# Optimization experiments

Hardware: AMD Instinct MI355X
Metric: run time of the kernel (lower is better)

The kernel has to match this reference:

```python
import jax, jax.numpy as jnp
import numpy as np

B, T, C = 256, 512, 128


def setup_inputs() -> dict:
    key = jax.random.key(0)
    k1, k2, k3 = jax.random.split(key, 3)
    inputs = jax.random.normal(k1, (B, T, C), dtype=jnp.float32)
    # learned transition matrix (orthogonal init approximated by scaled normal)
    transitions = jax.random.normal(k2, (C, C), dtype=jnp.float32) * 0.1
    # variable sequence lengths in [T//2, T] -> keras-style boolean mask
    lengths = jax.random.randint(k3, (B,), T // 2, T + 1)
    mask = jnp.arange(T)[None, :] < lengths[:, None]  # [B, T] bool
    return {"inputs": inputs, "mask": mask, "transitions": transitions}


def reference(inputs, mask, transitions):
    # Faithful port of CRF.call: sequence_lengths from mask, then Viterbi decode
    # (tfa.text.crf_decode): max-plus forward DP with backpointers + backtrack.
    Bn, Tn, Cn = inputs.shape
    seq_len = jnp.sum(mask.astype(jnp.int32), axis=-1)  # [B]

    ident = jnp.arange(Cn, dtype=jnp.int32)[None, :]  # identity backpointer row

    def fwd_step(state, xs):
        # state: [B, C] best score ending in each tag
        pot_t, valid = xs  # [B, C], [B] bool
        scores = state[:, :, None] + transitions[None]      # [B, Cprev, Ccur]
        new_state = jnp.max(scores, axis=1) + pot_t          # [B, C]
        bp = jnp.argmax(scores, axis=1).astype(jnp.int32)    # [B, C]
        state = jnp.where(valid[:, None], new_state, state)  # carry past length
        bp = jnp.where(valid[:, None], bp, ident)            # identity beyond length
        return state, bp

    pots = jnp.swapaxes(inputs[:, 1:], 0, 1)  # [T-1, B, C]
    valid = mask[:, 1:].T                      # [T-1, B]
    state, bps = jax.lax.scan(fwd_step, inputs[:, 0], (pots, valid))

    last_tag = jnp.argmax(state, axis=-1).astype(jnp.int32)  # [B]

    def bwd_step(tag, bp_t):
        prev = jnp.take_along_axis(bp_t, tag[:, None], axis=1)[:, 0]
        return prev, prev

    _, tags_rest = jax.lax.scan(bwd_step, last_tag, bps, reverse=True)  # [T-1, B]
    viterbi = jnp.concatenate([tags_rest, last_tag[None]], axis=0).T    # [B, T]
    return viterbi, inputs, seq_len, transitions
```

## Files before the change

### kernel.cpp

```cpp
#include <hip/hip_runtime.h>


#define BB 256
#define TT 512
#define CC 128
#define NTH 1024
#define GR 8
#define JP 16
#define SPAD 20

#define OFF_VIT 0
#define OFF_INP (BB * TT)
#define OFF_LEN (OFF_INP + BB * TT * CC)
#define OFF_TR (OFF_LEN + BB)

#define BP_BYTES ((TT - 1) * CC)
#define STATE_FLOATS (2 * GR * SPAD)
#define SMEM_BYTES (BP_BYTES + STATE_FLOATS * 4 + 16 * 4 + 16)

template <int CTRL>
__device__ __forceinline__ void dpp_first_max(float& v, int& bi) {
  float ov = __int_as_float(__builtin_amdgcn_update_dpp(0, __float_as_int(v), CTRL, 0xF, 0xF, true));
  int oi = __builtin_amdgcn_update_dpp(0, bi, CTRL, 0xF, 0xF, true);
  bool take = (ov > v) || (ov == v && oi < bi);
  v = take ? ov : v;
  bi = take ? oi : bi;
}

#define CHAIN(VNAME, JIDX, BACC, IACC)              \
  {                                                 \
    float VNAME = sjv + tr[JIDX];                   \
    if (VNAME > BACC) { BACC = VNAME; IACC = JIDX; } \
  }

__global__ __launch_bounds__(NTH, 1) void crf_viterbi(
    const float* __restrict__ inputs, const unsigned char* __restrict__ mask_bytes,
    const float* __restrict__ trans, float* __restrict__ out) {
  extern __shared__ unsigned char smem[];
  unsigned char* bp_s = smem;
  float* state_s = (float*)(smem + BP_BYTES);
  int* wsum = (int*)(state_s + STATE_FLOATS);

  const int b = blockIdx.x;
  const int tid = threadIdx.x;
  const int lane = tid & 63;
  const int wave = tid >> 6;
  const int ccur = tid >> 3;
  const int g = tid & 7;

  const int w4 = (mask_bytes[1] == 0) ? 4 : 1;
  if (tid < TT) {
    int mb = mask_bytes[(size_t)(b * TT + tid) * (size_t)w4] != 0;
    unsigned long long bal = __ballot(mb);
    if (lane == 0) wsum[wave] = __popcll(bal);
  }

  float tr[JP];
#pragma unroll
  for (int j = 0; j < JP; ++j) tr[j] = trans[(g * JP + j) * CC + ccur];

  const float* pin = inputs + (size_t)b * TT * CC;

  if (tid < CC) state_s[(tid >> 4) * SPAD + (tid & 15)] = pin[tid];
  __syncthreads();

  int L = 0;
#pragma unroll
  for (int i = 0; i < 8; ++i) L += wsum[i];

  float pot = pin[CC + ccur];
  int par = 0;

  for (int t = 1; t < L; ++t) {
    const float4* sp = (const float4*)(state_s + par * (GR * SPAD) + g * SPAD);
    float4 a0 = sp[0], a1 = sp[1], a2 = sp[2], a3 = sp[3];

    int tn = (t + 1 < L) ? (t + 1) : t;
    float potN = pin[tn * CC + ccur];

    float b0 = a0.x + tr[0]; int i0 = 0;
    float b1 = a0.y + tr[1]; int i1 = 1;
    { float sjv = a0.z; CHAIN(v2, 2, b0, i0) }
    { float sjv = a0.w; CHAIN(v3, 3, b1, i1) }
    { float sjv = a1.x; CHAIN(v4, 4, b0, i0) }
    { float sjv = a1.y; CHAIN(v5, 5, b1, i1) }
    { float sjv = a1.z; CHAIN(v6, 6, b0, i0) }
    { float sjv = a1.w; CHAIN(v7, 7, b1, i1) }
    { float sjv = a2.x; CHAIN(v8, 8, b0, i0) }
    { float sjv = a2.y; CHAIN(v9, 9, b1, i1) }
    { float sjv = a2.z; CHAIN(vA, 10, b0, i0) }
    { float sjv = a2.w; CHAIN(vB, 11, b1, i1) }
    { float sjv = a3.x; CHAIN(vC, 12, b0, i0) }
    { float sjv = a3.y; CHAIN(vD, 13, b1, i1) }
    { float sjv = a3.z; CHAIN(vE, 14, b0, i0) }
    { float sjv = a3.w; CHAIN(vF, 15, b1, i1) }

    bool t1 = (b1 > b0) || (b1 == b0 && i1 < i0);
    float v = t1 ? b1 : b0;
    int bi = (t1 ? i1 : i0) + g * JP;

    dpp_first_max<0xB1>(v, bi);
    dpp_first_max<0x4E>(v, bi);
    dpp_first_max<0x141>(v, bi);

    v += pot;

    if (g == 0) {
      state_s[(par ^ 1) * (GR * SPAD) + (ccur >> 4) * SPAD + (ccur & 15)] = v;
      bp_s[(t - 1) * CC + ccur] = (unsigned char)bi;
    }
    pot = potN;
    __syncthreads();
    par ^= 1;
  }

  if (wave == 0) {
    const float* fs = state_s + par * (GR * SPAD);
    float v1 = fs[(lane >> 4) * SPAD + (lane & 15)];
    int c2 = lane + 64;
    float v2 = fs[(c2 >> 4) * SPAD + (c2 & 15)];
    float v;
    int idx;
    if (v2 > v1) { v = v2; idx = c2; } else { v = v1; idx = lane; }
#pragma unroll
    for (int off = 32; off; off >>= 1) {
      float ov = __shfl_xor(v, off);
      int oi = __shfl_xor(idx, off);
      if (ov > v || (ov == v && oi < idx)) { v = ov; idx = oi; }
    }
    for (int t2 = L - 1 + lane; t2 < TT; t2 += 64) out[OFF_VIT + b * TT + t2] = (float)idx;
    if (lane == 0) {
      int cur = idx;
      for (int tt = L - 2; tt >= 0; --tt) {
        cur = bp_s[tt * CC + cur];
        out[OFF_VIT + b * TT + tt] = (float)cur;
      }
      out[OFF_LEN + b] = (float)L;
    }
  } else {
    if (wave == 1) out[OFF_TR + b * 64 + lane] = trans[b * 64 + lane];
    const float4* src = (const float4*)pin;
    float4* dst = (float4*)(out + OFF_INP + (size_t)b * TT * CC);
    for (int i = tid - 64; i < TT * CC / 4; i += NTH - 64) dst[i] = src[i];
  }
}

extern "C" void kernel_launch(void* const* d_in, const int* in_sizes, int n_in,
                              void* d_out, int out_size, void* d_ws, size_t ws_size,
                              hipStream_t stream) {
  const float* inputs = (const float*)d_in[0];
  const unsigned char* mask = (const unsigned char*)d_in[1];
  const float* trans = (const float*)d_in[2];
  float* out = (float*)d_out;

  crf_viterbi<<<BB, NTH, SMEM_BYTES, stream>>>(inputs, mask, trans, out);
}
```

Measured before the change: 501.9 us.

## Drop backpointer argmax from forward pass; recompute path from stored scores

The forward DP now computes only the max over previous tags, with no argmax index tracking. Each step's state vector goes to a global history buffer (workspace, or the output's input slot as fallback). The backtrack recomputes each argmax from the stored scores plus a transposed transition matrix in shared memory, using a wave-wide butterfly, and prefetches history rows ahead. This shortens the serial per-step critical path at the cost of global writes every step and a heavier serial backtrack. It also replaces __syncthreads with a raw lgkmcnt wait plus barrier.

```diff
diff --git a/kernel.cpp b/kernel.cpp
--- a/kernel.cpp
+++ b/kernel.cpp
@@ -14,31 +14,45 @@
 #define OFF_LEN (OFF_INP + BB * TT * CC)
 #define OFF_TR (OFF_LEN + BB)
 
-#define BP_BYTES ((TT - 1) * CC)
+#define TRT_FLOATS (CC * CC)
 #define STATE_FLOATS (2 * GR * SPAD)
-#define SMEM_BYTES (BP_BYTES + STATE_FLOATS * 4 + 16 * 4 + 16)
+#define SMEM_BYTES ((TRT_FLOATS + STATE_FLOATS + 16) * 4 + 16)
 
-template <int CTRL>
-__device__ __forceinline__ void dpp_first_max(float& v, int& bi) {
-  float ov = __int_as_float(__builtin_amdgcn_update_dpp(0, __float_as_int(v), CTRL, 0xF, 0xF, true));
-  int oi = __builtin_amdgcn_update_dpp(0, bi, CTRL, 0xF, 0xF, true);
-  bool take = (ov > v) || (ov == v && oi < bi);
-  v = take ? ov : v;
-  bi = take ? oi : bi;
+#define F3(a, b, c) fmaxf(fmaxf((a), (b)), (c))
+
+template <int C>
+__device__ __forceinline__ float dppmaxf(float v) {
+  float o = __int_as_float(__builtin_amdgcn_update_dpp(0, __float_as_int(v), C, 0xF, 0xF, true));
+  return fmaxf(v, o);
 }
 
-#define CHAIN(VNAME, JIDX, BACC, IACC)              \
-  {                                                 \
-    float VNAME = sjv + tr[JIDX];                   \
-    if (VNAME > BACC) { BACC = VNAME; IACC = JIDX; } \
-  }
+__device__ __forceinline__ void lexmax(float& v, int& i, float ov, int oi) {
+  bool take = (ov > v) || (ov == v && oi < i);
+  v = take ? ov : v;
+  i = take ? oi : i;
+}
+template <int C>
+__device__ __forceinline__ void bfly_dpp(float& v, int& i) {
+  float ov = __int_as_float(__builtin_amdgcn_update_dpp(0, __float_as_int(v), C, 0xF, 0xF, true));
+  int oi = __builtin_amdgcn_update_dpp(0, i, C, 0xF, 0xF, true);
+  lexmax(v, i, ov, oi);
+}
+__device__ __forceinline__ void bfly6(float& v, int& i) {
+  bfly_dpp<0xB1>(v, i);
+  bfly_dpp<0x4E>(v, i);
+  bfly_dpp<0x141>(v, i);
+  bfly_dpp<0x140>(v, i);
+  { float ov = __shfl_xor(v, 16); int oi = __shfl_xor(i, 16); lexmax(v, i, ov, oi); }
+  { float ov = __shfl_xor(v, 32); int oi = __shfl_xor(i, 32); lexmax(v, i, ov, oi); }
+}
 
 __global__ __launch_bounds__(NTH, 1) void crf_viterbi(
     const float* __restrict__ inputs, const unsigned char* __restrict__ mask_bytes,
-    const float* __restrict__ trans, float* __restrict__ out) {
-  extern __shared__ unsigned char smem[];
-  unsigned char* bp_s = smem;
-  float* state_s = (float*)(smem + BP_BYTES);
+    const float* __restrict__ trans, float* __restrict__ out,
+    float* __restrict__ hist, int useWs) {
+  extern __shared__ float smemf[];
+  float* trT = smemf;
+  float* state_s = smemf + TRT_FLOATS;
   int* wsum = (int*)(state_s + STATE_FLOATS);
 
   const int b = blockIdx.x;
@@ -55,13 +69,32 @@
     if (lane == 0) wsum[wave] = __popcll(bal);
   }
 
+  {
+    const float4* tsrc = (const float4*)(trans + tid * 16);
+    float4 q0 = tsrc[0], q1 = tsrc[1], q2 = tsrc[2], q3 = tsrc[3];
+    int p = tid >> 3, c0 = (tid & 7) * 16;
+    trT[(c0 + 0) * CC + p] = q0.x;  trT[(c0 + 1) * CC + p] = q0.y;
+    trT[(c0 + 2) * CC + p] = q0.z;  trT[(c0 + 3) * CC + p] = q0.w;
+    trT[(c0 + 4) * CC + p] = q1.x;  trT[(c0 + 5) * CC + p] = q1.y;
+    trT[(c0 + 6) * CC + p] = q1.z;  trT[(c0 + 7) * CC + p] = q1.w;
+    trT[(c0 + 8) * CC + p] = q2.x;  trT[(c0 + 9) * CC + p] = q2.y;
+    trT[(c0 + 10) * CC + p] = q2.z; trT[(c0 + 11) * CC + p] = q2.w;
+    trT[(c0 + 12) * CC + p] = q3.x; trT[(c0 + 13) * CC + p] = q3.y;
+    trT[(c0 + 14) * CC + p] = q3.z; trT[(c0 + 15) * CC + p] = q3.w;
+  }
+
   float tr[JP];
 #pragma unroll
   for (int j = 0; j < JP; ++j) tr[j] = trans[(g * JP + j) * CC + ccur];
 
   const float* pin = inputs + (size_t)b * TT * CC;
+  float* hist_b = hist + (size_t)b * TT * CC;
 
-  if (tid < CC) state_s[(tid >> 4) * SPAD + (tid & 15)] = pin[tid];
+  if (tid < CC) {
+    float x0 = pin[tid];
+    state_s[(tid >> 4) * SPAD + (tid & 15)] = x0;
+    hist_b[tid] = x0;
+  }
   __syncthreads();
 
   int L = 0;
@@ -78,66 +111,66 @@
     int tn = (t + 1 < L) ? (t + 1) : t;
     float potN = pin[tn * CC + ccur];
 
-    float b0 = a0.x + tr[0]; int i0 = 0;
-    float b1 = a0.y + tr[1]; int i1 = 1;
-    { float sjv = a0.z; CHAIN(v2, 2, b0, i0) }
-    { float sjv = a0.w; CHAIN(v3, 3, b1, i1) }
-    { float sjv = a1.x; CHAIN(v4, 4, b0, i0) }
-    { float sjv = a1.y; CHAIN(v5, 5, b1, i1) }
-    { float sjv = a1.z; CHAIN(v6, 6, b0, i0) }
-    { float sjv = a1.w; CHAIN(v7, 7, b1, i1) }
-    { float sjv = a2.x; CHAIN(v8, 8, b0, i0) }
-    { float sjv = a2.y; CHAIN(v9, 9, b1, i1) }
-    { float sjv = a2.z; CHAIN(vA, 10, b0, i0) }
-    { float sjv = a2.w; CHAIN(vB, 11, b1, i1) }
-    { float sjv = a3.x; CHAIN(vC, 12, b0, i0) }
-    { float sjv = a3.y; CHAIN(vD, 13, b1, i1) }
-    { float sjv = a3.z; CHAIN(vE, 14, b0, i0) }
-    { float sjv = a3.w; CHAIN(vF, 15, b1, i1) }
+    float t0 = a0.x + tr[0], t1 = a0.y + tr[1], t2 = a0.z + tr[2], t3 = a0.w + tr[3];
+    float t4 = a1.x + tr[4], t5 = a1.y + tr[5], t6 = a1.z + tr[6], t7 = a1.w + tr[7];
+    float t8 = a2.x + tr[8], t9 = a2.y + tr[9], tA = a2.z + tr[10], tB = a2.w + tr[11];
+    float tC = a3.x + tr[12], tD = a3.y + tr[13], tE = a3.z + tr[14], tF = a3.w + tr[15];
 
-    bool t1 = (b1 > b0) || (b1 == b0 && i1 < i0);
-    float v = t1 ? b1 : b0;
-    int bi = (t1 ? i1 : i0) + g * JP;
-
-    dpp_first_max<0xB1>(v, bi);
-    dpp_first_max<0x4E>(v, bi);
-    dpp_first_max<0x141>(v, bi);
-
-    v += pot;
+    float m = fmaxf(F3(F3(t0, t1, t2), F3(t3, t4, t5), F3(t6, t7, t8)),
+                    F3(F3(t9, tA, tB), F3(tC, tD, tE), tF));
+    m = dppmaxf<0xB1>(m);
+    m = dppmaxf<0x4E>(m);
+    m = dppmaxf<0x141>(m);
+    float v = m + pot;
 
     if (g == 0) {
       state_s[(par ^ 1) * (GR * SPAD) + (ccur >> 4) * SPAD + (ccur & 15)] = v;
-      bp_s[(t - 1) * CC + ccur] = (unsigned char)bi;
+      hist_b[t * CC + ccur] = v;
     }
     pot = potN;
-    __syncthreads();
+    asm volatile("s_waitcnt lgkmcnt(0)\n\ts_barrier" ::: "memory");
     par ^= 1;
   }
 
+  __syncthreads();
+
+  float* outv = out + OFF_VIT + b * TT;
+
   if (wave == 0) {
     const float* fs = state_s + par * (GR * SPAD);
-    float v1 = fs[(lane >> 4) * SPAD + (lane & 15)];
-    int c2 = lane + 64;
-    float v2 = fs[(c2 >> 4) * SPAD + (c2 & 15)];
-    float v;
-    int idx;
-    if (v2 > v1) { v = v2; idx = c2; } else { v = v1; idx = lane; }
-#pragma unroll
-    for (int off = 32; off; off >>= 1) {
-      float ov = __shfl_xor(v, off);
-      int oi = __shfl_xor(idx, off);
-      if (ov > v || (ov == v && oi < idx)) { v = ov; idx = oi; }
+    int p0 = 2 * lane;
+    float2 sv = *(const float2*)&fs[(p0 >> 4) * SPAD + (p0 & 15)];
+    float v = sv.x;
+    int bi = p0;
+    if (sv.y > v) { v = sv.y; bi = p0 + 1; }
+    bfly6(v, bi);
+
+    for (int t2 = L - 1 + lane; t2 < TT; t2 += 64) outv[t2] = (float)bi;
+    if (lane == 0) out[OFF_LEN + b] = (float)L;
+
+    int cur = bi;
+    float2 r0 = *(const float2*)(hist_b + (size_t)(L - 2) * CC + p0);
+    float2 r1 = *(const float2*)(hist_b + (size_t)(L >= 3 ? L - 3 : 0) * CC + p0);
+    float2 r2 = *(const float2*)(hist_b + (size_t)(L >= 4 ? L - 4 : 0) * CC + p0);
+    for (int t = L - 1; t >= 1; --t) {
+      float2 w = *(const float2*)&trT[cur * CC + p0];
+      float s0 = r0.x + w.x, s1 = r0.y + w.y;
+      float vv = s0;
+      int ii = p0;
+      if (s1 > vv) { vv = s1; ii = p0 + 1; }
+      bfly6(vv, ii);
+      cur = ii;
+      if (lane == 0) outv[t - 1] = (float)cur;
+      r0 = r1; r1 = r2;
+      int tp = t - 4;
+      if (tp < 0) tp = 0;
+      r2 = *(const float2*)(hist_b + (size_t)tp * CC + p0);
     }
-    for (int t2 = L - 1 + lane; t2 < TT; t2 += 64) out[OFF_VIT + b * TT + t2] = (float)idx;
-    if (lane == 0) {
-      int cur = idx;
-      for (int tt = L - 2; tt >= 0; --tt) {
-        cur = bp_s[tt * CC + cur];
-        out[OFF_VIT + b * TT + tt] = (float)cur;
-      }
-      out[OFF_LEN + b] = (float)L;
-    }
-  } else {
+  }
+
+  if (!useWs) __syncthreads();
+
+  if (wave != 0) {
     if (wave == 1) out[OFF_TR + b * 64 + lane] = trans[b * 64 + lane];
     const float4* src = (const float4*)pin;
     float4* dst = (float4*)(out + OFF_INP + (size_t)b * TT * CC);
@@ -153,5 +186,9 @@
   const float* trans = (const float*)d_in[2];
   float* out = (float*)d_out;
 
-  crf_viterbi<<<BB, NTH, SMEM_BYTES, stream>>>(inputs, mask, trans, out);
+  const size_t need = (size_t)BB * TT * CC * sizeof(float);
+  int useWs = (ws_size >= need) ? 1 : 0;
+  float* hist = useWs ? (float*)d_ws : (out + OFF_INP);
+
+  crf_viterbi<<<BB, NTH, SMEM_BYTES, stream>>>(inputs, mask, trans, out, hist, useWs);
 }
```

After: 706.6 us. +40.8%, slower.

## Split Viterbi argmax into max-reduce then index-match, lighten barrier

Applied to the files above, without the earlier changes.

Replaces the per-element compare-and-track argmax chain with a tree of fmaxf for the max value, a DPP max across the 8-lane group, then a second pass that finds the lowest index equal to the max and a DPP min-reduce on indices. This shortens the serial dependency chain in the per-timestep critical path. The __syncthreads is replaced with an explicit lgkmcnt wait plus s_barrier, and potential loads are limited to the writer lanes. The final argmax butterfly uses DPP steps for the low offsets. Tie-breaking relies on exact float equality, which matches the reference's first-index semantics.

```diff
diff --git a/kernel.cpp b/kernel.cpp
--- a/kernel.cpp
+++ b/kernel.cpp
@@ -18,20 +18,38 @@
 #define STATE_FLOATS (2 * GR * SPAD)
 #define SMEM_BYTES (BP_BYTES + STATE_FLOATS * 4 + 16 * 4 + 16)
 
-template <int CTRL>
-__device__ __forceinline__ void dpp_first_max(float& v, int& bi) {
-  float ov = __int_as_float(__builtin_amdgcn_update_dpp(0, __float_as_int(v), CTRL, 0xF, 0xF, true));
-  int oi = __builtin_amdgcn_update_dpp(0, bi, CTRL, 0xF, 0xF, true);
-  bool take = (ov > v) || (ov == v && oi < bi);
-  v = take ? ov : v;
-  bi = take ? oi : bi;
+#define F3(a, b, c) fmaxf(fmaxf((a), (b)), (c))
+
+template <int C>
+__device__ __forceinline__ float dppmaxf(float v) {
+  float o = __int_as_float(__builtin_amdgcn_update_dpp(0, __float_as_int(v), C, 0xF, 0xF, true));
+  return fmaxf(v, o);
+}
+template <int C>
+__device__ __forceinline__ unsigned dppminu(unsigned v) {
+  unsigned o = (unsigned)__builtin_amdgcn_update_dpp(0, (int)v, C, 0xF, 0xF, true);
+  return v < o ? v : o;
 }
 
-#define CHAIN(VNAME, JIDX, BACC, IACC)              \
-  {                                                 \
-    float VNAME = sjv + tr[JIDX];                   \
-    if (VNAME > BACC) { BACC = VNAME; IACC = JIDX; } \
-  }
+__device__ __forceinline__ void lexmax(float& v, int& i, float ov, int oi) {
+  bool take = (ov > v) || (ov == v && oi < i);
+  v = take ? ov : v;
+  i = take ? oi : i;
+}
+template <int C>
+__device__ __forceinline__ void bfly_dpp(float& v, int& i) {
+  float ov = __int_as_float(__builtin_amdgcn_update_dpp(0, __float_as_int(v), C, 0xF, 0xF, true));
+  int oi = __builtin_amdgcn_update_dpp(0, i, C, 0xF, 0xF, true);
+  lexmax(v, i, ov, oi);
+}
+__device__ __forceinline__ void bfly6(float& v, int& i) {
+  bfly_dpp<0xB1>(v, i);
+  bfly_dpp<0x4E>(v, i);
+  bfly_dpp<0x141>(v, i);
+  bfly_dpp<0x140>(v, i);
+  { float ov = __shfl_xor(v, 16); int oi = __shfl_xor(i, 16); lexmax(v, i, ov, oi); }
+  { float ov = __shfl_xor(v, 32); int oi = __shfl_xor(i, 32); lexmax(v, i, ov, oi); }
+}
 
 __global__ __launch_bounds__(NTH, 1) void crf_viterbi(
     const float* __restrict__ inputs, const unsigned char* __restrict__ mask_bytes,
@@ -47,6 +65,7 @@
   const int wave = tid >> 6;
   const int ccur = tid >> 3;
   const int g = tid & 7;
+  const bool g0 = (g == 0);
 
   const int w4 = (mask_bytes[1] == 0) ? 4 : 1;
   if (tid < TT) {
@@ -68,7 +87,7 @@
 #pragma unroll
   for (int i = 0; i < 8; ++i) L += wsum[i];
 
-  float pot = pin[CC + ccur];
+  float pot = g0 ? pin[CC + ccur] : 0.f;
   int par = 0;
 
   for (int t = 1; t < L; ++t) {
@@ -76,43 +95,44 @@
     float4 a0 = sp[0], a1 = sp[1], a2 = sp[2], a3 = sp[3];
 
     int tn = (t + 1 < L) ? (t + 1) : t;
-    float potN = pin[tn * CC + ccur];
+    float potN = 0.f;
+    if (g0) potN = pin[tn * CC + ccur];
 
-    float b0 = a0.x + tr[0]; int i0 = 0;
-    float b1 = a0.y + tr[1]; int i1 = 1;
-    { float sjv = a0.z; CHAIN(v2, 2, b0, i0) }
-    { float sjv = a0.w; CHAIN(v3, 3, b1, i1) }
-    { float sjv = a1.x; CHAIN(v4, 4, b0, i0) }
-    { float sjv = a1.y; CHAIN(v5, 5, b1, i1) }
-    { float sjv = a1.z; CHAIN(v6, 6, b0, i0) }
-    { float sjv = a1.w; CHAIN(v7, 7, b1, i1) }
-    { float sjv = a2.x; CHAIN(v8, 8, b0, i0) }
-    { float sjv = a2.y; CHAIN(v9, 9, b1, i1) }
-    { float sjv = a2.z; CHAIN(vA, 10, b0, i0) }
-    { float sjv = a2.w; CHAIN(vB, 11, b1, i1) }
-    { float sjv = a3.x; CHAIN(vC, 12, b0, i0) }
-    { float sjv = a3.y; CHAIN(vD, 13, b1, i1) }
-    { float sjv = a3.z; CHAIN(vE, 14, b0, i0) }
-    { float sjv = a3.w; CHAIN(vF, 15, b1, i1) }
+    float t0 = a0.x + tr[0], t1 = a0.y + tr[1], t2 = a0.z + tr[2], t3 = a0.w + tr[3];
+    float t4 = a1.x + tr[4], t5 = a1.y + tr[5], t6 = a1.z + tr[6], t7 = a1.w + tr[7];
+    float t8 = a2.x + tr[8], t9 = a2.y + tr[9], tA = a2.z + tr[10], tB = a2.w + tr[11];
+    float tC = a3.x + tr[12], tD = a3.y + tr[13], tE = a3.z + tr[14], tF = a3.w + tr[15];
 
-    bool t1 = (b1 > b0) || (b1 == b0 && i1 < i0);
-    float v = t1 ? b1 : b0;
-    int bi = (t1 ? i1 : i0) + g * JP;
+    float m = fmaxf(F3(F3(t0, t1, t2), F3(t3, t4, t5), F3(t6, t7, t8)),
+                    F3(F3(t9, tA, tB), F3(tC, tD, tE), tF));
+    m = dppmaxf<0xB1>(m);
+    m = dppmaxf<0x4E>(m);
+    m = dppmaxf<0x141>(m);
 
-    dpp_first_max<0xB1>(v, bi);
-    dpp_first_max<0x4E>(v, bi);
-    dpp_first_max<0x141>(v, bi);
+    unsigned iA = 255u, iB = 255u;
+    iA = (t7 == m) ? 7u : iA;  iB = (tF == m) ? 15u : iB;
+    iA = (t6 == m) ? 6u : iA;  iB = (tE == m) ? 14u : iB;
+    iA = (t5 == m) ? 5u : iA;  iB = (tD == m) ? 13u : iB;
+    iA = (t4 == m) ? 4u : iA;  iB = (tC == m) ? 12u : iB;
+    iA = (t3 == m) ? 3u : iA;  iB = (tB == m) ? 11u : iB;
+    iA = (t2 == m) ? 2u : iA;  iB = (tA == m) ? 10u : iB;
+    iA = (t1 == m) ? 1u : iA;  iB = (t9 == m) ? 9u : iB;
+    iA = (t0 == m) ? 0u : iA;  iB = (t8 == m) ? 8u : iB;
+    unsigned bi = ((iA != 255u) ? iA : iB) + (unsigned)(g * JP);
+    bi = dppminu<0xB1>(bi);
+    bi = dppminu<0x4E>(bi);
+    bi = dppminu<0x141>(bi);
 
-    v += pot;
-
-    if (g == 0) {
-      state_s[(par ^ 1) * (GR * SPAD) + (ccur >> 4) * SPAD + (ccur & 15)] = v;
+    if (g0) {
+      state_s[(par ^ 1) * (GR * SPAD) + (ccur >> 4) * SPAD + (ccur & 15)] = m + pot;
       bp_s[(t - 1) * CC + ccur] = (unsigned char)bi;
     }
     pot = potN;
-    __syncthreads();
+    asm volatile("s_waitcnt lgkmcnt(0)\n\ts_barrier" ::: "memory");
     par ^= 1;
   }
+
+  float* outv = out + OFF_VIT + b * TT;
 
   if (wave == 0) {
     const float* fs = state_s + par * (GR * SPAD);
@@ -122,20 +142,16 @@
     float v;
     int idx;
     if (v2 > v1) { v = v2; idx = c2; } else { v = v1; idx = lane; }
-#pragma unroll
-    for (int off = 32; off; off >>= 1) {
-      float ov = __shfl_xor(v, off);
-      int oi = __shfl_xor(idx, off);
-      if (ov > v || (ov == v && oi < idx)) { v = ov; idx = oi; }
-    }
-    for (int t2 = L - 1 + lane; t2 < TT; t2 += 64) out[OFF_VIT + b * TT + t2] = (float)idx;
+    bfly6(v, idx);
+
+    for (int t2 = L - 1 + lane; t2 < TT; t2 += 64) outv[t2] = (float)idx;
     if (lane == 0) {
+      out[OFF_LEN + b] = (float)L;
       int cur = idx;
       for (int tt = L - 2; tt >= 0; --tt) {
         cur = bp_s[tt * CC + cur];
-        out[OFF_VIT + b * TT + tt] = (float)cur;
+        outv[tt] = (float)cur;
       }
-      out[OFF_LEN + b] = (float)L;
     }
   } else {
     if (wave == 1) out[OFF_TR + b * 64 + lane] = trans[b * 64 + lane];
```

New measurement: 440.3 us. 12.3% less time.
